# Optimization experiments

Hardware: AMD Instinct MI355X
Metric: run time of the kernel (lower is better)

## Reference

```python
import jax, jax.numpy as jnp
import numpy as np

N_NODES = 100000
N_EDGES = 1000000
N_LABEL = 200000
D_IN = 64
D_HID = 64


def setup_inputs() -> dict:
    key = jax.random.key(0)
    ks = jax.random.split(key, 9)
    s = 1.0 / np.sqrt(D_IN)
    return {
        "x": jax.random.normal(ks[0], (N_NODES, D_IN), jnp.float32),
        "edge_index": jax.random.randint(ks[1], (2, N_EDGES), 0, N_NODES, jnp.int64),
        "edge_label_index": jax.random.randint(ks[2], (2, N_LABEL), 0, N_NODES, jnp.int64),
        "W1_l": jax.random.normal(ks[3], (D_IN, D_HID), jnp.float32) * s,
        "W1_r": jax.random.normal(ks[4], (D_IN, D_HID), jnp.float32) * s,
        "b1": jnp.zeros((D_HID,), jnp.float32),
        "W2_l": jax.random.normal(ks[5], (D_HID, D_HID), jnp.float32) * s,
        "W2_r": jax.random.normal(ks[6], (D_HID, D_HID), jnp.float32) * s,
        "b2": jnp.zeros((D_HID,), jnp.float32),
    }


def _sage_conv(x, edge_index, W_l, W_r, b):
    # PyG SAGEConv with mean aggregation: out = mean_agg @ W_l + b + x @ W_r
    src, dst = edge_index[0], edge_index[1]
    n = x.shape[0]
    # gather source features, scatter-sum into destination nodes
    agg = jax.ops.segment_sum(x[src], dst, num_segments=n)          # [N, D]
    cnt = jax.ops.segment_sum(jnp.ones(src.shape, x.dtype), dst, num_segments=n)
    mean = agg / jnp.maximum(cnt, 1.0)[:, None]
    return mean @ W_l + x @ W_r + b


def reference(x, edge_index, edge_label_index, W1_l, W1_r, b1, W2_l, W2_r, b2):
    h = jax.nn.relu(_sage_conv(x, edge_index, W1_l, W1_r, b1))
    z = _sage_conv(h, edge_index, W2_l, W2_r, b2)
    # dot-product edge decode
    src_e = z[edge_label_index[0]]  # [E_label, D]
    dst_e = z[edge_label_index[1]]
    return jnp.sum(src_e * dst_e, axis=-1)  # [E_label]
```

## Files before the change

kernel.cpp:

```cpp
#include <hip/hip_runtime.h>

#define D 64
#define NB_SHIFT 9
#define NODES_PER_B 512
#define CAP1 12288

typedef __attribute__((ext_vector_type(8))) short short8;
typedef __attribute__((ext_vector_type(4))) float f32x4;

__device__ inline unsigned short f2bf(float f) {
    unsigned int u = __float_as_uint(f);
    return (unsigned short)((u + 0x7FFFu + ((u >> 16) & 1u)) >> 16);
}
__device__ inline float bf2f(unsigned short s) {
    return __uint_as_float(((unsigned int)s) << 16);
}

__global__ void f32_to_bf16_kernel(const float* __restrict__ in,
                                   unsigned short* __restrict__ outp, int n4) {
    int i = blockIdx.x * blockDim.x + threadIdx.x;
    int stride = gridDim.x * blockDim.x;
    for (int t = i; t < n4; t += stride) {
        float4 v = ((const float4*)in)[t];
        ushort4 o;
        o.x = f2bf(v.x); o.y = f2bf(v.y); o.z = f2bf(v.z); o.w = f2bf(v.w);
        ((ushort4*)outp)[t] = o;
    }
}

__global__ __launch_bounds__(256) void bin_edges_kernel(
        const int* __restrict__ src, const int* __restrict__ dst,
        int* __restrict__ gcount, int* __restrict__ binned,
        int n_edges, int n_buckets) {
    __shared__ int lhist[256];
    __shared__ int lbase[256];
    int tid = threadIdx.x;
    int per = (n_edges + gridDim.x - 1) / gridDim.x;
    int beg = blockIdx.x * per;
    int end = min(beg + per, n_edges);

    lhist[tid] = 0;
    __syncthreads();
    for (int e = beg + tid; e < end; e += 256)
        atomicAdd(&lhist[dst[e] >> NB_SHIFT], 1);
    __syncthreads();
    if (tid < n_buckets && lhist[tid] > 0)
        lbase[tid] = atomicAdd(&gcount[tid], lhist[tid]);
    else
        lbase[tid] = 0;
    __syncthreads();
    lhist[tid] = 0;
    __syncthreads();
    for (int e = beg + tid; e < end; e += 256) {
        int d = dst[e];
        int b = d >> NB_SHIFT;
        int off = lbase[b] + atomicAdd(&lhist[b], 1);
        if (off < CAP1)
            binned[(size_t)b * CAP1 + off] =
                (src[e] << NB_SHIFT) | (d & (NODES_PER_B - 1));
    }
}

__global__ __launch_bounds__(256) void build_csr_kernel(
        const int* __restrict__ binned, const int* __restrict__ gcount,
        int* __restrict__ rowp, int* __restrict__ ssrc,
        int n_nodes, int n_buckets, int n_edges) {
    __shared__ int lhist[NODES_PER_B];
    __shared__ int lbase[NODES_PER_B];
    __shared__ int tmp[256];
    __shared__ int stage[CAP1];

    int b   = blockIdx.x;
    int tid = threadIdx.x;

    int v = (tid < n_buckets) ? min(gcount[tid], CAP1) : 0;
    tmp[tid] = v;
    __syncthreads();
    for (int off = 1; off < 256; off <<= 1) {
        int t = 0;
        if (tid >= off) t = tmp[tid - off];
        __syncthreads();
        if (tid >= off) tmp[tid] += t;
        __syncthreads();
    }
    int base = (b == 0) ? 0 : tmp[b - 1];
    int cnt  = min(gcount[b], CAP1);
    if (b == 0 && tid == 0) rowp[n_nodes] = n_edges;
    __syncthreads();

    int nodebase = b << NB_SHIFT;
    int nlocal   = min(NODES_PER_B, n_nodes - nodebase);
    const int* ebuf = binned + (size_t)b * CAP1;

    lhist[tid] = 0;
    lhist[tid + 256] = 0;
    __syncthreads();
    for (int i = tid; i < cnt; i += 256)
        atomicAdd(&lhist[ebuf[i] & (NODES_PER_B - 1)], 1);
    __syncthreads();

    int a0 = lhist[2 * tid];
    int a1 = lhist[2 * tid + 1];
    tmp[tid] = a0 + a1;
    __syncthreads();
    for (int off = 1; off < 256; off <<= 1) {
        int t = 0;
        if (tid >= off) t = tmp[tid - off];
        __syncthreads();
        if (tid >= off) tmp[tid] += t;
        __syncthreads();
    }
    int excl = tmp[tid] - (a0 + a1);
    lbase[2 * tid]     = excl;
    lbase[2 * tid + 1] = excl + a0;
    __syncthreads();

    for (int j = tid; j < nlocal; j += 256)
        rowp[nodebase + j] = base + lbase[j];

    lhist[tid] = 0;
    lhist[tid + 256] = 0;
    __syncthreads();

    for (int i = tid; i < cnt; i += 256) {
        int e  = ebuf[i];
        int ln = e & (NODES_PER_B - 1);
        int off = atomicAdd(&lhist[ln], 1);
        stage[lbase[ln] + off] = e >> NB_SHIFT;
    }
    __syncthreads();

    for (int i = tid; i < cnt; i += 256)
        ssrc[base + i] = stage[i];
}

__global__ void pack_w4_kernel(const float* __restrict__ W0,
                               const float* __restrict__ W1,
                               const float* __restrict__ W2,
                               const float* __restrict__ W3,
                               unsigned short* __restrict__ pw) {
    int idx = blockIdx.x * blockDim.x + threadIdx.x;
    if (idx >= 4 * 4096) return;
    int m = idx >> 12;
    int r = idx & 4095;
    const float* W = (m == 0) ? W0 : (m == 1) ? W1 : (m == 2) ? W2 : W3;
    int j    = r & 7;
    int lane = (r >> 3) & 63;
    int kk   = (r >> 9) & 1;
    int ct   = r >> 10;
    int k    = kk * 32 + ((lane >> 4) & 3) * 8 + j;
    int col  = ct * 16 + (lane & 15);
    pw[idx] = f2bf(W[k * D + col]);
}

__global__ __launch_bounds__(256) void aggregate_bf16_kernel(
        const unsigned short* __restrict__ feat,
        const int* __restrict__ row_ptr,
        const int* __restrict__ sorted_src,
        unsigned short* __restrict__ mean_out,
        int n_nodes) {
    int lane = threadIdx.x & 63;
    int r    = lane >> 4;
    int c    = lane & 15;
    int wave   = (int)((blockIdx.x * blockDim.x + threadIdx.x) >> 6);
    int nwaves = (int)((gridDim.x * blockDim.x) >> 6);
    int npw  = (n_nodes + nwaves - 1) / nwaves;
    int nbeg = wave * npw;
    int nend = min(nbeg + npw, n_nodes);
    if (nbeg >= nend) return;

    int beg = row_ptr[nbeg];
    for (int node = nbeg; node < nend; ++node) {
        int end = row_ptr[node + 1];
        int endm1 = end - 1;
        float a0 = 0.f, a1 = 0.f, a2 = 0.f, a3 = 0.f;

        for (int i = beg; i < end; i += 16) {
            int e0 = i + r, e1 = i + 4 + r, e2 = i + 8 + r, e3 = i + 12 + r;
            int s0 = sorted_src[min(e0, endm1)];
            int s1 = sorted_src[min(e1, endm1)];
            int s2 = sorted_src[min(e2, endm1)];
            int s3 = sorted_src[min(e3, endm1)];
            ushort4 v0 = *(const ushort4*)(feat + ((size_t)s0 << 6) + (c << 2));
            ushort4 v1 = *(const ushort4*)(feat + ((size_t)s1 << 6) + (c << 2));
            ushort4 v2 = *(const ushort4*)(feat + ((size_t)s2 << 6) + (c << 2));
            ushort4 v3 = *(const ushort4*)(feat + ((size_t)s3 << 6) + (c << 2));
            if (e0 < end) {
                a0 += bf2f(v0.x); a1 += bf2f(v0.y);
                a2 += bf2f(v0.z); a3 += bf2f(v0.w);
            }
            if (e1 < end) {
                a0 += bf2f(v1.x); a1 += bf2f(v1.y);
                a2 += bf2f(v1.z); a3 += bf2f(v1.w);
            }
            if (e2 < end) {
                a0 += bf2f(v2.x); a1 += bf2f(v2.y);
                a2 += bf2f(v2.z); a3 += bf2f(v2.w);
            }
            if (e3 < end) {
                a0 += bf2f(v3.x); a1 += bf2f(v3.y);
                a2 += bf2f(v3.z); a3 += bf2f(v3.w);
            }
        }
        a0 += __shfl_xor(a0, 16); a1 += __shfl_xor(a1, 16);
        a2 += __shfl_xor(a2, 16); a3 += __shfl_xor(a3, 16);
        a0 += __shfl_xor(a0, 32); a1 += __shfl_xor(a1, 32);
        a2 += __shfl_xor(a2, 32); a3 += __shfl_xor(a3, 32);

        float inv = 1.0f / (float)max(end - beg, 1);
        if (r == 0) {
            ushort4 o;
            o.x = f2bf(a0 * inv); o.y = f2bf(a1 * inv);
            o.z = f2bf(a2 * inv); o.w = f2bf(a3 * inv);
            *(ushort4*)(mean_out + ((size_t)node << 6) + (c << 2)) = o;
        }
        beg = end;
    }
}

__global__ __launch_bounds__(256) void sage_linear_mfma_kernel(
        const unsigned short* __restrict__ mean,
        const unsigned short* __restrict__ xin,
        const unsigned short* __restrict__ pwl,
        const unsigned short* __restrict__ pwr,
        const float* __restrict__ bias,
        unsigned short* __restrict__ outp,
        int n_nodes, int do_relu) {
    int lane = threadIdx.x & 63;
    int wid  = threadIdx.x >> 6;
    int arow = lane & 15;
    int kgrp = lane >> 4;

    short8 wl[4][2], wr[4][2];
#pragma unroll
    for (int ct = 0; ct < 4; ++ct)
#pragma unroll
        for (int kk = 0; kk < 2; ++kk) {
            wl[ct][kk] = *(const short8*)(pwl + (((ct * 2 + kk) * 64 + lane) << 3));
            wr[ct][kk] = *(const short8*)(pwr + (((ct * 2 + kk) * 64 + lane) << 3));
        }
    float bj[4];
#pragma unroll
    for (int ct = 0; ct < 4; ++ct) bj[ct] = bias[ct * 16 + arow];

    int wave   = blockIdx.x * 4 + wid;
    int nwaves = gridDim.x * 4;
    int ntiles = (n_nodes + 15) >> 4;

    for (int t = wave; t < ntiles; t += nwaves) {
        int base = t * 16;
        int lrow = base + arow;
        if (lrow >= n_nodes) lrow = n_nodes - 1;
        const unsigned short* mrow = mean + (size_t)lrow * D + kgrp * 8;
        const unsigned short* xrow = xin  + (size_t)lrow * D + kgrp * 8;
        short8 am0 = *(const short8*)(mrow);
        short8 am1 = *(const short8*)(mrow + 32);
        short8 ax0 = *(const short8*)(xrow);
        short8 ax1 = *(const short8*)(xrow + 32);

#pragma unroll
        for (int ct = 0; ct < 4; ++ct) {
            f32x4 acc = {0.f, 0.f, 0.f, 0.f};
            acc = __builtin_amdgcn_mfma_f32_16x16x32_bf16(am0, wl[ct][0], acc, 0, 0, 0);
            acc = __builtin_amdgcn_mfma_f32_16x16x32_bf16(am1, wl[ct][1], acc, 0, 0, 0);
            acc = __builtin_amdgcn_mfma_f32_16x16x32_bf16(ax0, wr[ct][0], acc, 0, 0, 0);
            acc = __builtin_amdgcn_mfma_f32_16x16x32_bf16(ax1, wr[ct][1], acc, 0, 0, 0);
            int col = ct * 16 + arow;
#pragma unroll
            for (int rr = 0; rr < 4; ++rr) {
                int row = base + kgrp * 4 + rr;
                float v = acc[rr] + bj[ct];
                if (do_relu) v = fmaxf(v, 0.0f);
                if (row < n_nodes) outp[(size_t)row * D + col] = f2bf(v);
            }
        }
    }
}

__global__ __launch_bounds__(256) void decode_bf16_kernel(
        const unsigned short* __restrict__ z,
        const int* __restrict__ esrc,
        const int* __restrict__ edst,
        float* __restrict__ out,
        int n) {
    int lane = threadIdx.x & 63;
    int g    = lane >> 4;
    int c    = lane & 15;
    int wave   = (int)((blockIdx.x * blockDim.x + threadIdx.x) >> 6);
    int nwaves = (int)((gridDim.x * blockDim.x) >> 6);
    int niter  = (n + 3) >> 2;

    for (int it = wave; it < niter; it += nwaves) {
        int e  = it * 4 + g;
        int ec = min(e, n - 1);
        int s  = esrc[ec];
        int d0 = edst[ec];
        ushort4 vs = *(const ushort4*)(z + ((size_t)s  << 6) + (c << 2));
        ushort4 vd = *(const ushort4*)(z + ((size_t)d0 << 6) + (c << 2));
        float p = bf2f(vs.x) * bf2f(vd.x) + bf2f(vs.y) * bf2f(vd.y) +
                  bf2f(vs.z) * bf2f(vd.z) + bf2f(vs.w) * bf2f(vd.w);
        p += __shfl_xor(p, 1);
        p += __shfl_xor(p, 2);
        p += __shfl_xor(p, 4);
        p += __shfl_xor(p, 8);
        if (c == 0 && e < n) out[e] = p;
    }
}

extern "C" void kernel_launch(void* const* d_in, const int* in_sizes, int n_in,
                              void* d_out, int out_size, void* d_ws, size_t ws_size,
                              hipStream_t stream) {
    const float* x   = (const float*)d_in[0];
    const int*   ei  = (const int*)d_in[1];
    const int*   eli = (const int*)d_in[2];
    const float* W1l = (const float*)d_in[3];
    const float* W1r = (const float*)d_in[4];
    const float* b1  = (const float*)d_in[5];
    const float* W2l = (const float*)d_in[6];
    const float* W2r = (const float*)d_in[7];
    const float* b2  = (const float*)d_in[8];
    float* out = (float*)d_out;

    const int n_nodes = in_sizes[0] / D;
    const int n_edges = in_sizes[1] / 2;
    const int n_label = in_sizes[2] / 2;
    const int n_buckets = (n_nodes + NODES_PER_B - 1) >> NB_SHIFT;

    const int* e_src = ei;
    const int* e_dst = ei + n_edges;
    const int* l_src = eli;
    const int* l_dst = eli + n_label;

    unsigned short* xb    = (unsigned short*)d_ws;
    unsigned short* meanb = xb + (size_t)n_nodes * D;
    unsigned short* h     = meanb + (size_t)n_nodes * D;
    unsigned short* z     = h + (size_t)n_nodes * D;
    int* rowp   = (int*)(z + (size_t)n_nodes * D);
    int* ssrc   = rowp + (n_nodes + 1);
    int* gcount = ssrc + n_edges + 8;
    unsigned short* pw = (unsigned short*)(gcount + 256);
    unsigned short* pw1l = pw;
    unsigned short* pw1r = pw + 4096;
    unsigned short* pw2l = pw + 8192;
    unsigned short* pw2r = pw + 12288;
    int* binned = (int*)h;

    dim3 blk(256);
    dim3 grd_nodes(2048);
    dim3 grd_linear(512);

    f32_to_bf16_kernel<<<grd_nodes, blk, 0, stream>>>(x, xb, n_nodes * D / 4);
    pack_w4_kernel<<<dim3(64), blk, 0, stream>>>(W1l, W1r, W2l, W2r, pw);

    hipMemsetAsync(gcount, 0, 256 * sizeof(int), stream);
    bin_edges_kernel<<<dim3(512), blk, 0, stream>>>(e_src, e_dst, gcount, binned,
                                                    n_edges, n_buckets);
    build_csr_kernel<<<dim3(n_buckets), blk, 0, stream>>>(binned, gcount, rowp,
                                                          ssrc, n_nodes,
                                                          n_buckets, n_edges);

    aggregate_bf16_kernel<<<grd_nodes, blk, 0, stream>>>(xb, rowp, ssrc, meanb, n_nodes);
    sage_linear_mfma_kernel<<<grd_linear, blk, 0, stream>>>(meanb, xb, pw1l, pw1r, b1,
                                                            h, n_nodes, 1);

    aggregate_bf16_kernel<<<grd_nodes, blk, 0, stream>>>(h, rowp, ssrc, meanb, n_nodes);
    sage_linear_mfma_kernel<<<grd_linear, blk, 0, stream>>>(meanb, h, pw2l, pw2r, b2,
                                                            z, n_nodes, 0);

    decode_bf16_kernel<<<grd_nodes, blk, 0, stream>>>(z, l_src, l_dst, out, n_label);
}
```

Baseline: 144.9 us.

## Fuse neighbor aggregation into MFMA linear kernel and merge prep kernels

Each wave now gathers and averages neighbor features for its 16-node tile and stages the bf16 means in LDS, then feeds them straight to the MFMA linear layer. This removes the intermediate mean buffer and its global write and read-back in both layers. The x conversion, weight packing and gcount zeroing are merged into one prep kernel, replacing two launches and a memset. In exchange, aggregation parallelism changes: each 16-lane group walks one node's edges four at a time, so degree imbalance across the four nodes in a wave causes more divergence.

```diff
diff --git a/kernel.cpp b/kernel.cpp
--- a/kernel.cpp
+++ b/kernel.cpp
@@ -4,6 +4,7 @@
 #define NB_SHIFT 9
 #define NODES_PER_B 512
 #define CAP1 12288
+#define LDS_STRIDE 72
 
 typedef __attribute__((ext_vector_type(8))) short short8;
 typedef __attribute__((ext_vector_type(4))) float f32x4;
@@ -16,15 +17,32 @@
     return __uint_as_float(((unsigned int)s) << 16);
 }
 
-__global__ void f32_to_bf16_kernel(const float* __restrict__ in,
-                                   unsigned short* __restrict__ outp, int n4) {
-    int i = blockIdx.x * blockDim.x + threadIdx.x;
+__global__ __launch_bounds__(256) void prep_kernel(
+        const float* __restrict__ x, unsigned short* __restrict__ xb, int n4,
+        const float* __restrict__ W1l, const float* __restrict__ W1r,
+        const float* __restrict__ W2l, const float* __restrict__ W2r,
+        unsigned short* __restrict__ pw, int* __restrict__ gcount) {
+    int gid = blockIdx.x * blockDim.x + threadIdx.x;
     int stride = gridDim.x * blockDim.x;
-    for (int t = i; t < n4; t += stride) {
-        float4 v = ((const float4*)in)[t];
+    for (int t = gid; t < n4; t += stride) {
+        float4 v = ((const float4*)x)[t];
         ushort4 o;
         o.x = f2bf(v.x); o.y = f2bf(v.y); o.z = f2bf(v.z); o.w = f2bf(v.w);
-        ((ushort4*)outp)[t] = o;
+        ((ushort4*)xb)[t] = o;
+    }
+    if (gid < 4 * 4096) {
+        int m = gid >> 12;
+        int r = gid & 4095;
+        const float* W = (m == 0) ? W1l : (m == 1) ? W1r : (m == 2) ? W2l : W2r;
+        int j    = r & 7;
+        int lane = (r >> 3) & 63;
+        int kk   = (r >> 9) & 1;
+        int ct   = r >> 10;
+        int k    = kk * 32 + ((lane >> 4) & 3) * 8 + j;
+        int col  = ct * 16 + (lane & 15);
+        pw[gid] = f2bf(W[k * D + col]);
+    } else if (gid < 4 * 4096 + 256) {
+        gcount[gid - 4 * 4096] = 0;
     }
 }
 
@@ -134,102 +152,21 @@
         ssrc[base + i] = stage[i];
 }
 
-__global__ void pack_w4_kernel(const float* __restrict__ W0,
-                               const float* __restrict__ W1,
-                               const float* __restrict__ W2,
-                               const float* __restrict__ W3,
-                               unsigned short* __restrict__ pw) {
-    int idx = blockIdx.x * blockDim.x + threadIdx.x;
-    if (idx >= 4 * 4096) return;
-    int m = idx >> 12;
-    int r = idx & 4095;
-    const float* W = (m == 0) ? W0 : (m == 1) ? W1 : (m == 2) ? W2 : W3;
-    int j    = r & 7;
-    int lane = (r >> 3) & 63;
-    int kk   = (r >> 9) & 1;
-    int ct   = r >> 10;
-    int k    = kk * 32 + ((lane >> 4) & 3) * 8 + j;
-    int col  = ct * 16 + (lane & 15);
-    pw[idx] = f2bf(W[k * D + col]);
-}
-
-__global__ __launch_bounds__(256) void aggregate_bf16_kernel(
+__global__ __launch_bounds__(256) void sage_fused_kernel(
         const unsigned short* __restrict__ feat,
-        const int* __restrict__ row_ptr,
-        const int* __restrict__ sorted_src,
-        unsigned short* __restrict__ mean_out,
-        int n_nodes) {
-    int lane = threadIdx.x & 63;
-    int r    = lane >> 4;
-    int c    = lane & 15;
-    int wave   = (int)((blockIdx.x * blockDim.x + threadIdx.x) >> 6);
-    int nwaves = (int)((gridDim.x * blockDim.x) >> 6);
-    int npw  = (n_nodes + nwaves - 1) / nwaves;
-    int nbeg = wave * npw;
-    int nend = min(nbeg + npw, n_nodes);
-    if (nbeg >= nend) return;
-
-    int beg = row_ptr[nbeg];
-    for (int node = nbeg; node < nend; ++node) {
-        int end = row_ptr[node + 1];
-        int endm1 = end - 1;
-        float a0 = 0.f, a1 = 0.f, a2 = 0.f, a3 = 0.f;
-
-        for (int i = beg; i < end; i += 16) {
-            int e0 = i + r, e1 = i + 4 + r, e2 = i + 8 + r, e3 = i + 12 + r;
-            int s0 = sorted_src[min(e0, endm1)];
-            int s1 = sorted_src[min(e1, endm1)];
-            int s2 = sorted_src[min(e2, endm1)];
-            int s3 = sorted_src[min(e3, endm1)];
-            ushort4 v0 = *(const ushort4*)(feat + ((size_t)s0 << 6) + (c << 2));
-            ushort4 v1 = *(const ushort4*)(feat + ((size_t)s1 << 6) + (c << 2));
-            ushort4 v2 = *(const ushort4*)(feat + ((size_t)s2 << 6) + (c << 2));
-            ushort4 v3 = *(const ushort4*)(feat + ((size_t)s3 << 6) + (c << 2));
-            if (e0 < end) {
-                a0 += bf2f(v0.x); a1 += bf2f(v0.y);
-                a2 += bf2f(v0.z); a3 += bf2f(v0.w);
-            }
-            if (e1 < end) {
-                a0 += bf2f(v1.x); a1 += bf2f(v1.y);
-                a2 += bf2f(v1.z); a3 += bf2f(v1.w);
-            }
-            if (e2 < end) {
-                a0 += bf2f(v2.x); a1 += bf2f(v2.y);
-                a2 += bf2f(v2.z); a3 += bf2f(v2.w);
-            }
-            if (e3 < end) {
-                a0 += bf2f(v3.x); a1 += bf2f(v3.y);
-                a2 += bf2f(v3.z); a3 += bf2f(v3.w);
-            }
-        }
-        a0 += __shfl_xor(a0, 16); a1 += __shfl_xor(a1, 16);
-        a2 += __shfl_xor(a2, 16); a3 += __shfl_xor(a3, 16);
-        a0 += __shfl_xor(a0, 32); a1 += __shfl_xor(a1, 32);
-        a2 += __shfl_xor(a2, 32); a3 += __shfl_xor(a3, 32);
-
-        float inv = 1.0f / (float)max(end - beg, 1);
-        if (r == 0) {
-            ushort4 o;
-            o.x = f2bf(a0 * inv); o.y = f2bf(a1 * inv);
-            o.z = f2bf(a2 * inv); o.w = f2bf(a3 * inv);
-            *(ushort4*)(mean_out + ((size_t)node << 6) + (c << 2)) = o;
-        }
-        beg = end;
-    }
-}
-
-__global__ __launch_bounds__(256) void sage_linear_mfma_kernel(
-        const unsigned short* __restrict__ mean,
-        const unsigned short* __restrict__ xin,
+        const int* __restrict__ rowp,
+        const int* __restrict__ ssrc,
         const unsigned short* __restrict__ pwl,
         const unsigned short* __restrict__ pwr,
         const float* __restrict__ bias,
         unsigned short* __restrict__ outp,
         int n_nodes, int do_relu) {
+    __shared__ unsigned short sMean[4][16][LDS_STRIDE];
+
     int lane = threadIdx.x & 63;
     int wid  = threadIdx.x >> 6;
-    int arow = lane & 15;
-    int kgrp = lane >> 4;
+    int r    = lane >> 4;
+    int c    = lane & 15;
 
     short8 wl[4][2], wr[4][2];
 #pragma unroll
@@ -241,7 +178,7 @@
         }
     float bj[4];
 #pragma unroll
-    for (int ct = 0; ct < 4; ++ct) bj[ct] = bias[ct * 16 + arow];
+    for (int ct = 0; ct < 4; ++ct) bj[ct] = bias[ct * 16 + c];
 
     int wave   = blockIdx.x * 4 + wid;
     int nwaves = gridDim.x * 4;
@@ -249,12 +186,54 @@
 
     for (int t = wave; t < ntiles; t += nwaves) {
         int base = t * 16;
-        int lrow = base + arow;
-        if (lrow >= n_nodes) lrow = n_nodes - 1;
-        const unsigned short* mrow = mean + (size_t)lrow * D + kgrp * 8;
-        const unsigned short* xrow = xin  + (size_t)lrow * D + kgrp * 8;
-        short8 am0 = *(const short8*)(mrow);
-        short8 am1 = *(const short8*)(mrow + 32);
+
+#pragma unroll
+        for (int sub = 0; sub < 4; ++sub) {
+            int node = base + sub * 4 + r;
+            float a0 = 0.f, a1 = 0.f, a2 = 0.f, a3 = 0.f;
+            int deg = 0;
+            if (node < n_nodes) {
+                int beg = rowp[node];
+                int end = rowp[node + 1];
+                deg = end - beg;
+                int endm1 = end - 1;
+                for (int i = beg; i < end; i += 4) {
+                    int s0 = ssrc[i];
+                    int s1 = ssrc[min(i + 1, endm1)];
+                    int s2 = ssrc[min(i + 2, endm1)];
+                    int s3 = ssrc[min(i + 3, endm1)];
+                    ushort4 v0 = *(const ushort4*)(feat + ((size_t)s0 << 6) + (c << 2));
+                    ushort4 v1 = *(const ushort4*)(feat + ((size_t)s1 << 6) + (c << 2));
+                    ushort4 v2 = *(const ushort4*)(feat + ((size_t)s2 << 6) + (c << 2));
+                    ushort4 v3 = *(const ushort4*)(feat + ((size_t)s3 << 6) + (c << 2));
+                    a0 += bf2f(v0.x); a1 += bf2f(v0.y);
+                    a2 += bf2f(v0.z); a3 += bf2f(v0.w);
+                    if (i + 1 < end) {
+                        a0 += bf2f(v1.x); a1 += bf2f(v1.y);
+                        a2 += bf2f(v1.z); a3 += bf2f(v1.w);
+                    }
+                    if (i + 2 < end) {
+                        a0 += bf2f(v2.x); a1 += bf2f(v2.y);
+                        a2 += bf2f(v2.z); a3 += bf2f(v2.w);
+                    }
+                    if (i + 3 < end) {
+                        a0 += bf2f(v3.x); a1 += bf2f(v3.y);
+                        a2 += bf2f(v3.z); a3 += bf2f(v3.w);
+                    }
+                }
+            }
+            float inv = 1.0f / (float)max(deg, 1);
+            ushort4 o;
+            o.x = f2bf(a0 * inv); o.y = f2bf(a1 * inv);
+            o.z = f2bf(a2 * inv); o.w = f2bf(a3 * inv);
+            *(ushort4*)(&sMean[wid][sub * 4 + r][c << 2]) = o;
+        }
+        asm volatile("s_waitcnt lgkmcnt(0)" ::: "memory");
+
+        short8 am0 = *(const short8*)(&sMean[wid][c][r * 8]);
+        short8 am1 = *(const short8*)(&sMean[wid][c][r * 8 + 32]);
+        int lrow = min(base + c, n_nodes - 1);
+        const unsigned short* xrow = feat + ((size_t)lrow << 6) + r * 8;
         short8 ax0 = *(const short8*)(xrow);
         short8 ax1 = *(const short8*)(xrow + 32);
 
@@ -265,10 +244,10 @@
             acc = __builtin_amdgcn_mfma_f32_16x16x32_bf16(am1, wl[ct][1], acc, 0, 0, 0);
             acc = __builtin_amdgcn_mfma_f32_16x16x32_bf16(ax0, wr[ct][0], acc, 0, 0, 0);
             acc = __builtin_amdgcn_mfma_f32_16x16x32_bf16(ax1, wr[ct][1], acc, 0, 0, 0);
-            int col = ct * 16 + arow;
+            int col = ct * 16 + c;
 #pragma unroll
             for (int rr = 0; rr < 4; ++rr) {
-                int row = base + kgrp * 4 + rr;
+                int row = base + r * 4 + rr;
                 float v = acc[rr] + bj[ct];
                 if (do_relu) v = fmaxf(v, 0.0f);
                 if (row < n_nodes) outp[(size_t)row * D + col] = f2bf(v);
@@ -331,10 +310,9 @@
     const int* l_src = eli;
     const int* l_dst = eli + n_label;
 
-    unsigned short* xb    = (unsigned short*)d_ws;
-    unsigned short* meanb = xb + (size_t)n_nodes * D;
-    unsigned short* h     = meanb + (size_t)n_nodes * D;
-    unsigned short* z     = h + (size_t)n_nodes * D;
+    unsigned short* xb = (unsigned short*)d_ws;
+    unsigned short* h  = xb + (size_t)n_nodes * D;
+    unsigned short* z  = h + (size_t)n_nodes * D;
     int* rowp   = (int*)(z + (size_t)n_nodes * D);
     int* ssrc   = rowp + (n_nodes + 1);
     int* gcount = ssrc + n_edges + 8;
@@ -346,26 +324,23 @@
     int* binned = (int*)h;
 
     dim3 blk(256);
-    dim3 grd_nodes(2048);
-    dim3 grd_linear(512);
-
-    f32_to_bf16_kernel<<<grd_nodes, blk, 0, stream>>>(x, xb, n_nodes * D / 4);
-    pack_w4_kernel<<<dim3(64), blk, 0, stream>>>(W1l, W1r, W2l, W2r, pw);
-
-    hipMemsetAsync(gcount, 0, 256 * sizeof(int), stream);
+
+    prep_kernel<<<dim3(2048), blk, 0, stream>>>(x, xb, n_nodes * D / 4,
+                                                W1l, W1r, W2l, W2r, pw, gcount);
+
     bin_edges_kernel<<<dim3(512), blk, 0, stream>>>(e_src, e_dst, gcount, binned,
                                                     n_edges, n_buckets);
     build_csr_kernel<<<dim3(n_buckets), blk, 0, stream>>>(binned, gcount, rowp,
                                                           ssrc, n_nodes,
                                                           n_buckets, n_edges);
 
-    aggregate_bf16_kernel<<<grd_nodes, blk, 0, stream>>>(xb, rowp, ssrc, meanb, n_nodes);
-    sage_linear_mfma_kernel<<<grd_linear, blk, 0, stream>>>(meanb, xb, pw1l, pw1r, b1,
-                                                            h, n_nodes, 1);
-
-    aggregate_bf16_kernel<<<grd_nodes, blk, 0, stream>>>(h, rowp, ssrc, meanb, n_nodes);
-    sage_linear_mfma_kernel<<<grd_linear, blk, 0, stream>>>(meanb, h, pw2l, pw2r, b2,
-                                                            z, n_nodes, 0);
-
-    decode_bf16_kernel<<<grd_nodes, blk, 0, stream>>>(z, l_src, l_dst, out, n_label);
-}
+    sage_fused_kernel<<<dim3(1024), blk, 0, stream>>>(xb, rowp, ssrc,
+                                                      pw1l, pw1r, b1, h,
+                                                      n_nodes, 1);
+
+    sage_fused_kernel<<<dim3(1024), blk, 0, stream>>>(h, rowp, ssrc,
+                                                      pw2l, pw2r, b2, z,
+                                                      n_nodes, 0);
+
+    decode_bf16_kernel<<<dim3(2048), blk, 0, stream>>>(z, l_src, l_dst, out, n_label);
+}
```

Result: slower. 158.1 us (+9.1%).
